# Kernel optimization log

Hardware: AMD Instinct MI355X
Metric: run time of the kernel (lower is better)

## Reference

```python
import jax, jax.numpy as jnp
import numpy as np

D_MODEL = 1024
NUM_HEADS = 16
LOCAL_WINDOW = 128
GLOBAL_STRIDE = 64
B, T = 4, 2048


def _rope_tables(T, d_head, base=10000.0):
    half = d_head // 2
    pos = jnp.arange(T, dtype=jnp.float32)[:, None]
    inv_freq = 1.0 / base ** (jnp.arange(half, dtype=jnp.float32) / half)
    ang = pos * inv_freq[None, :]  # (T, half)
    return jnp.cos(ang), jnp.sin(ang)


def _rope_apply(x, cos_h, sin_h):
    # x: (B, H, T, d_head), cos_h/sin_h: (T, d_head//2); interleaved pairs
    xe = x[..., 0::2]
    xo = x[..., 1::2]
    re = xe * cos_h - xo * sin_h
    ro = xe * sin_h + xo * cos_h
    return jnp.stack([re, ro], axis=-1).reshape(x.shape)


def setup_inputs() -> dict:
    key = jax.random.key(0)
    k1, k2, k3 = jax.random.split(key, 3)
    x = jax.random.normal(k1, (B, T, D_MODEL), dtype=jnp.float32)
    W_qkv = jax.random.normal(k2, (D_MODEL, 3 * D_MODEL), dtype=jnp.float32) * (D_MODEL ** -0.5)
    W_out = jax.random.normal(k3, (D_MODEL, D_MODEL), dtype=jnp.float32) * (D_MODEL ** -0.5)
    b_out = jnp.zeros((D_MODEL,), dtype=jnp.float32)
    return {"x": x, "W_qkv": W_qkv, "W_out": W_out, "b_out": b_out}


def reference(x, W_qkv, W_out, b_out):
    Bx, Tx, C = x.shape
    H = NUM_HEADS
    dh = C // H

    qkv = x @ W_qkv  # (B, T, 3C)
    qkv = qkv.reshape(Bx, Tx, 3, H, dh)
    q, k, v = qkv[:, :, 0], qkv[:, :, 1], qkv[:, :, 2]  # (B, T, H, dh)
    q = jnp.transpose(q, (0, 2, 1, 3))  # (B, H, T, dh)
    k = jnp.transpose(k, (0, 2, 1, 3))
    v = jnp.transpose(v, (0, 2, 1, 3))

    cos_h, sin_h = _rope_tables(Tx, dh)
    q = _rope_apply(q, cos_h, sin_h)
    k = _rope_apply(k, cos_h, sin_h)

    scores = jnp.einsum('bhtd,bhkd->bhtk', q, k) / jnp.sqrt(jnp.float32(dh))

    lw = min(LOCAL_WINDOW, Tx)
    gs = max(1, GLOBAL_STRIDE)
    q_idx = jnp.arange(Tx)
    k_idx = jnp.arange(Tx)
    rel = k_idx[None, :] - q_idx[:, None]  # (T, T)
    local_ok = (rel <= 0) & (rel >= -(lw - 1))
    key_global = (k_idx % gs == 0)[None, :]
    query_is_global = (q_idx % gs == 0)[:, None]
    allowed = (local_ok | key_global | query_is_global) & (rel <= 0)
    allowed = allowed[None, None, :, :]

    scores = jnp.where(allowed, scores, jnp.float32(-1e9))
    w = jax.nn.softmax(scores, axis=-1)
    out = jnp.einsum('bhtk,bhkd->bhtd', w, v)
    out = jnp.transpose(out, (0, 2, 1, 3)).reshape(Bx, Tx, C)
    return out @ W_out + b_out
```

## Files before the change

### kernel.cpp

```cpp
#include <hip/hip_runtime.h>
#include <cstdint>

#define DEV __device__ __forceinline__

typedef __bf16 bf16x8 __attribute__((ext_vector_type(8)));
typedef float f32x4 __attribute__((ext_vector_type(4)));
typedef float f32x16 __attribute__((ext_vector_type(16)));
typedef uint32_t u32x4 __attribute__((ext_vector_type(4)));

DEV uint16_t f2b(float f) {
  uint32_t u = __builtin_bit_cast(uint32_t, f);
  u = u + 0x7fffu + ((u >> 16) & 1u);
  return (uint16_t)(u >> 16);
}
DEV float b2f(uint16_t h) { return __builtin_bit_cast(float, (uint32_t)h << 16); }
DEV uint32_t pk2(float lo, float hi) {
  return (uint32_t)f2b(lo) | ((uint32_t)f2b(hi) << 16);
}

DEV f32x16 mfma32(bf16x8 a, bf16x8 b, f32x16 c) {
  return __builtin_amdgcn_mfma_f32_32x32x16_bf16(a, b, c, 0, 0, 0);
}

DEV void gload16(const void* g, void* s) {
  __builtin_amdgcn_global_load_lds((const __attribute__((address_space(1))) uint32_t*)g,
                                   (__attribute__((address_space(3))) uint32_t*)s, 16, 0, 0);
}

__global__ void k_convert_bf16(const float* __restrict__ X, uint16_t* __restrict__ Xb, int n4) {
  int i = blockIdx.x * 256 + threadIdx.x;
  if (i >= n4) return;
  float4 v = ((const float4*)X)[i];
  uint16_t o0 = f2b(v.x), o1 = f2b(v.y), o2 = f2b(v.z), o3 = f2b(v.w);
  uint64_t packed = (uint64_t)o0 | ((uint64_t)o1 << 16) | ((uint64_t)o2 << 32) | ((uint64_t)o3 << 48);
  ((uint64_t*)Xb)[i] = packed;
}

__global__ __launch_bounds__(256) void k_transpose_bf16(const float* __restrict__ W,
                                                        uint16_t* __restrict__ Wt, int R, int C) {
  __shared__ uint16_t sh[64][68];
  const int tid = threadIdx.x;
  const int bc = blockIdx.x * 64, br = blockIdx.y * 64;
#pragma unroll
  for (int it = 0; it < 16; ++it) {
    const int e = it * 256 + tid;
    const int i = e >> 6, j = e & 63;
    sh[j][i] = f2b(W[(size_t)(br + i) * C + bc + j]);
  }
  __syncthreads();
#pragma unroll
  for (int it = 0; it < 2; ++it) {
    const int e = it * 256 + tid;
    const int j = e >> 3, i8 = (e & 7) * 8;
    uint16_t tmp[8];
#pragma unroll
    for (int k = 0; k < 8; ++k) tmp[k] = sh[j][i8 + k];
    *(uint4*)&Wt[(size_t)(bc + j) * R + br + i8] = *(uint4*)tmp;
  }
}

__global__ void k_rope(float* __restrict__ rc, float* __restrict__ rs) {
  int idx = blockIdx.x * 256 + threadIdx.x;
  if (idx >= 2048 * 32) return;
  int t = idx >> 5, j = idx & 31;
  float inv = powf(10000.f, -(float)j / 32.f);
  float ang = (float)t * inv;
  rc[idx] = cosf(ang);
  rs[idx] = sinf(ang);
}

__global__ __launch_bounds__(256) void k_transpose_v(const uint16_t* __restrict__ V,
                                                     uint16_t* __restrict__ Vt) {
  __shared__ uint16_t sh[64][72];
  const int tid = threadIdx.x;
  const int bh = blockIdx.x >> 5;
  const int t0 = (blockIdx.x & 31) * 64;
#pragma unroll
  for (int it = 0; it < 2; ++it) {
    const int idx = it * 256 + tid;
    const int tr = idx >> 3, d8 = (idx & 7) * 8;
    uint4 vv = *(const uint4*)&V[((size_t)(bh << 11) + t0 + tr) * 64 + d8];
    const uint16_t* e = (const uint16_t*)&vv;
#pragma unroll
    for (int j = 0; j < 8; ++j) sh[d8 + j][tr] = e[j];
  }
  __syncthreads();
#pragma unroll
  for (int it = 0; it < 2; ++it) {
    const int idx = it * 256 + tid;
    const int d = idx >> 3, t8 = (idx & 7) * 8;
    uint16_t tmp[8];
#pragma unroll
    for (int j = 0; j < 8; ++j) tmp[j] = sh[d][t8 + j];
    *(uint4*)&Vt[((size_t)bh * 64 + d) * 2048 + t0 + t8] = *(uint4*)tmp;
  }
}

__global__ __launch_bounds__(256) void k_gather(const uint16_t* __restrict__ Qd,
                                                const uint16_t* __restrict__ Kd,
                                                const uint16_t* __restrict__ Vt,
                                                uint16_t* __restrict__ Qg,
                                                uint16_t* __restrict__ Kg,
                                                uint16_t* __restrict__ Vtg) {
  const int tid = threadIdx.x;
  const int bh = blockIdx.x;
  {
    const int g = tid >> 3, d8 = (tid & 7) * 8;
    const size_t src = ((size_t)(bh << 11) + g * 64) * 64 + d8;
    const size_t dst = ((size_t)bh * 32 + g) * 64 + d8;
    *(uint4*)&Kg[dst] = *(const uint4*)&Kd[src];
    *(uint4*)&Qg[dst] = *(const uint4*)&Qd[src];
  }
  {
    const int d = tid >> 2, g8 = (tid & 3) * 8;
    uint16_t tmp[8];
#pragma unroll
    for (int j = 0; j < 8; ++j) tmp[j] = Vt[((size_t)bh * 64 + d) * 2048 + (size_t)(g8 + j) * 64];
    *(uint4*)&Vtg[((size_t)bh * 64 + d) * 32 + g8] = *(uint4*)tmp;
  }
}

template <int MODE>
__global__ __launch_bounds__(256) void gemm32(
    const uint16_t* __restrict__ A, const uint16_t* __restrict__ Bt,
    int M, int N, int K,
    uint16_t* __restrict__ Qd, uint16_t* __restrict__ Kd, uint16_t* __restrict__ Vd,
    const float* __restrict__ rc, const float* __restrict__ rs,
    float* __restrict__ Cout, const float* __restrict__ bias) {
  __shared__ __align__(16) uint16_t sA[128 * 64];
  __shared__ __align__(16) uint16_t sB[128 * 64];
  const int tid = threadIdx.x;
  const int w = tid >> 6, lane = tid & 63;
  const int wm = w >> 1, wn = w & 1;
  const int ln = lane & 31, hi = lane >> 5;
  const int bm = blockIdx.y * 128, bn = blockIdx.x * 128;

  f32x16 acc[2][2] = {};

  const int lsw = (ln & 7) << 4;

  for (int kt = 0; kt < K; kt += 64) {
#pragma unroll
    for (int r = 0; r < 4; ++r) {
      const int slot = r * 256 + tid;
      const int row = slot >> 3, c8 = slot & 7;
      const int gc = kt + ((c8 ^ (row & 7)) << 3);
      gload16(A + (size_t)(bm + row) * K + gc, (char*)sA + (r * 256 + (tid & ~63)) * 16);
      gload16(Bt + (size_t)(bn + row) * K + gc, (char*)sB + (r * 256 + (tid & ~63)) * 16);
    }
    __syncthreads();
#pragma unroll
    for (int ks = 0; ks < 4; ++ks) {
      const int cb = ks * 32 + hi * 16;
      bf16x8 af[2], bf[2];
#pragma unroll
      for (int mi = 0; mi < 2; ++mi) {
        const int row = wm * 64 + mi * 32 + ln;
        af[mi] = *(const bf16x8*)((const char*)sA + row * 128 + (cb ^ lsw));
      }
#pragma unroll
      for (int ni = 0; ni < 2; ++ni) {
        const int row = wn * 64 + ni * 32 + ln;
        bf[ni] = *(const bf16x8*)((const char*)sB + row * 128 + (cb ^ lsw));
      }
#pragma unroll
      for (int mi = 0; mi < 2; ++mi)
#pragma unroll
        for (int ni = 0; ni < 2; ++ni)
          acc[mi][ni] = mfma32(af[mi], bf[ni], acc[mi][ni]);
    }
    __syncthreads();
  }

#pragma unroll
  for (int mi = 0; mi < 2; ++mi) {
#pragma unroll
    for (int ni = 0; ni < 2; ++ni) {
      const int colb = bn + wn * 64 + ni * 32 + ln;
#pragma unroll
      for (int r = 0; r < 16; ++r) {
        const int crow = (r & 3) + 8 * (r >> 2) + 4 * hi;
        const int row = bm + wm * 64 + mi * 32 + crow;
        float val = acc[mi][ni][r];
        if (MODE == 0) {
          const int b = row >> 11, t = row & 2047;
          const float pv = __shfl_xor(val, 1);
          if (colb < 2048) {
            const int d = colb & 63, j = d >> 1;
            const float c = rc[t * 32 + j], s = rs[t * 32 + j];
            const float rv = (d & 1) ? (val * c + pv * s) : (val * c - pv * s);
            const int cc = colb & 1023, h = cc >> 6;
            uint16_t* dst = (colb < 1024) ? Qd : Kd;
            dst[((((size_t)b * 16 + h) * 2048 + t) << 6) + d] = f2b(rv);
          } else {
            const int cc = colb - 2048;
            const int h = cc >> 6, d = cc & 63;
            Vd[((((size_t)b * 16 + h) * 2048 + t) << 6) + d] = f2b(val);
          }
        } else {
          Cout[(size_t)row * N + colb] = val + bias[colb];
        }
      }
    }
  }
}

template <int MASK>
DEV void attn_tile(const uint16_t* __restrict__ kb_ptr, const uint16_t* __restrict__ v_ptr,
                   const int vrs, const int kb, const int qv, const int hi, const int ln,
                   const bf16x8 qf[4], float& m, float& l, f32x16& acc0, f32x16& acc1) {
  bf16x8 kf0 = *(const bf16x8*)&kb_ptr[ln * 64 + 0 + hi * 8];
  bf16x8 kf1 = *(const bf16x8*)&kb_ptr[ln * 64 + 16 + hi * 8];
  bf16x8 kf2 = *(const bf16x8*)&kb_ptr[ln * 64 + 32 + hi * 8];
  bf16x8 kf3 = *(const bf16x8*)&kb_ptr[ln * 64 + 48 + hi * 8];
  bf16x8 vf00 = *(const bf16x8*)&v_ptr[ln * vrs + hi * 8];
  bf16x8 vf01 = *(const bf16x8*)&v_ptr[ln * vrs + 16 + hi * 8];
  bf16x8 vf10 = *(const bf16x8*)&v_ptr[(32 + ln) * vrs + hi * 8];
  bf16x8 vf11 = *(const bf16x8*)&v_ptr[(32 + ln) * vrs + 16 + hi * 8];

  f32x16 sv = {};
  sv = mfma32(kf0, qf[0], sv);
  sv = mfma32(kf1, qf[1], sv);
  sv = mfma32(kf2, qf[2], sv);
  sv = mfma32(kf3, qf[3], sv);

  float s[16];
  float pm = -3.0e38f;
#pragma unroll
  for (int r = 0; r < 16; ++r) {
    const int crow = (r & 3) + 8 * (r >> 2) + 4 * hi;
    bool ok;
    if (MASK == 0) {
      const int key = kb + crow;
      ok = (key <= qv) && (key + 127 >= qv);
    } else if (MASK == 1) {
      ok = crow * 64 <= qv - 128;
    } else {
      const int key = kb + crow;
      ok = (key <= qv);
    }
    s[r] = ok ? sv[r] * 0.125f : -3.0e38f;
    pm = fmaxf(pm, s[r]);
  }
  pm = fmaxf(pm, __shfl_xor(pm, 32));

  if (__any(pm > m + 8.0f)) {
    const float mn = fmaxf(m, pm);
    const float f = __expf(m - mn);
#pragma unroll
    for (int r = 0; r < 16; ++r) {
      const int crow = (r & 3) + 8 * (r >> 2) + 4 * hi;
      const float fr = __shfl(f, crow);
      acc0[r] *= fr;
      acc1[r] *= fr;
    }
    l *= f;
    m = mn;
  }

  float p[16];
  float ps = 0.f;
#pragma unroll
  for (int r = 0; r < 16; ++r) {
    p[r] = __expf(s[r] - m);
    ps += p[r];
  }
  l += ps + __shfl_xor(ps, 32);

  const uint32_t q0a = pk2(p[0], p[1]), q0b = pk2(p[2], p[3]);
  const uint32_t q1a = pk2(p[4], p[5]), q1b = pk2(p[6], p[7]);
  const uint32_t q2a = pk2(p[8], p[9]), q2b = pk2(p[10], p[11]);
  const uint32_t q3a = pk2(p[12], p[13]), q3b = pk2(p[14], p[15]);
  const uint32_t p0a = __shfl_xor(q0a, 32), p0b = __shfl_xor(q0b, 32);
  const uint32_t p1a = __shfl_xor(q1a, 32), p1b = __shfl_xor(q1b, 32);
  const uint32_t p2a = __shfl_xor(q2a, 32), p2b = __shfl_xor(q2b, 32);
  const uint32_t p3a = __shfl_xor(q3a, 32), p3b = __shfl_xor(q3b, 32);
  u32x4 f0, f1;
  f0[0] = hi ? p1a : q0a; f0[1] = hi ? p1b : q0b; f0[2] = hi ? q1a : p0a; f0[3] = hi ? q1b : p0b;
  f1[0] = hi ? p3a : q2a; f1[1] = hi ? p3b : q2b; f1[2] = hi ? q3a : p2a; f1[3] = hi ? q3b : p2b;
  const bf16x8 pa0 = __builtin_bit_cast(bf16x8, f0);
  const bf16x8 pa1 = __builtin_bit_cast(bf16x8, f1);

  acc0 = mfma32(pa0, vf00, acc0);
  acc0 = mfma32(pa1, vf01, acc0);
  acc1 = mfma32(pa0, vf10, acc1);
  acc1 = mfma32(pa1, vf11, acc1);
}

__global__ __launch_bounds__(256) void attn_main(const uint16_t* __restrict__ Qd,
                                                 const uint16_t* __restrict__ Kd,
                                                 const uint16_t* __restrict__ Vt,
                                                 const uint16_t* __restrict__ Kg,
                                                 const uint16_t* __restrict__ Vtg,
                                                 uint16_t* __restrict__ O) {
  const int tid = threadIdx.x;
  const int wid = blockIdx.x * 4 + (tid >> 6);
  const int bh = wid >> 6, qt = wid & 63;
  const int qb = qt * 32;
  const int lane = tid & 63, hi = lane >> 5, ln = lane & 31;
  const int qv = qb + ln;

  bf16x8 qf[4];
#pragma unroll
  for (int i = 0; i < 4; ++i)
    qf[i] = *(const bf16x8*)&Qd[((size_t)(bh << 11) + qv) * 64 + i * 16 + hi * 8];

  float m = -1e30f, l = 0.f;
  f32x16 acc0 = {}, acc1 = {};

  const int kb0 = qb >= 128 ? qb - 128 : 0;
  for (int kbb = kb0; kbb <= qb; kbb += 32)
    attn_tile<0>(Kd + ((size_t)(bh << 11) + kbb) * 64, Vt + (size_t)bh * 64 * 2048 + kbb, 2048,
                 kbb, qv, hi, ln, qf, m, l, acc0, acc1);
  if (qb >= 128)
    attn_tile<1>(Kg + (size_t)bh * 32 * 64, Vtg + (size_t)bh * 64 * 32, 32,
                 0, qv, hi, ln, qf, m, l, acc0, acc1);

  const float linv = 1.0f / l;
  const int b = bh >> 4, h = bh & 15;
  const int ocol = h * 64 + ln;
#pragma unroll
  for (int r = 0; r < 16; ++r) {
    const int crow = (r & 3) + 8 * (r >> 2) + 4 * hi;
    const float sc = __shfl(linv, crow);
    const size_t orow = (size_t)(b * 2048 + qb + crow);
    O[orow * 1024 + ocol] = f2b(acc0[r] * sc);
    O[orow * 1024 + ocol + 32] = f2b(acc1[r] * sc);
  }
}

__global__ __launch_bounds__(256) void attn_global(const uint16_t* __restrict__ Qg,
                                                   const uint16_t* __restrict__ Kd,
                                                   const uint16_t* __restrict__ Vt,
                                                   uint16_t* __restrict__ O) {
  __shared__ float accL[4][32][64];
  __shared__ float mL[4][32];
  __shared__ float lL[4][32];
  const int tid = threadIdx.x;
  const int bh = blockIdx.x;
  const int wv = tid >> 6, lane = tid & 63, hi = lane >> 5, ln = lane & 31;
  const int qv = ln * 64;

  bf16x8 qf[4];
#pragma unroll
  for (int i = 0; i < 4; ++i)
    qf[i] = *(const bf16x8*)&Qg[((size_t)bh * 32 + ln) * 64 + i * 16 + hi * 8];

  float m = -1e30f, l = 0.f;
  f32x16 acc0 = {}, acc1 = {};
  for (int kt = wv; kt < 64; kt += 4) {
    const int kbb = kt * 32;
    attn_tile<2>(Kd + ((size_t)(bh << 11) + kbb) * 64, Vt + (size_t)bh * 64 * 2048 + kbb, 2048,
                 kbb, qv, hi, ln, qf, m, l, acc0, acc1);
  }

  if (hi == 0) {
    mL[wv][ln] = m;
    lL[wv][ln] = l;
  }
#pragma unroll
  for (int r = 0; r < 16; ++r) {
    const int crow = (r & 3) + 8 * (r >> 2) + 4 * hi;
    accL[wv][crow][ln] = acc0[r];
    accL[wv][crow][ln + 32] = acc1[r];
  }
  __syncthreads();

  const int q = tid >> 3, d0 = (tid & 7) * 8;
  float M = fmaxf(fmaxf(mL[0][q], mL[1][q]), fmaxf(mL[2][q], mL[3][q]));
  float L = 0.f;
  float v[8] = {};
#pragma unroll
  for (int w = 0; w < 4; ++w) {
    const float ew = __expf(mL[w][q] - M);
    L += lL[w][q] * ew;
#pragma unroll
    for (int j = 0; j < 8; ++j) v[j] += accL[w][q][d0 + j] * ew;
  }
  const float Li = 1.0f / L;
  const int b = bh >> 4, h = bh & 15;
  const size_t orow = (size_t)(b * 2048 + q * 64);
#pragma unroll
  for (int j = 0; j < 8; ++j) O[orow * 1024 + h * 64 + d0 + j] = f2b(v[j] * Li);
}

extern "C" void kernel_launch(void* const* d_in, const int* in_sizes, int n_in,
                              void* d_out, int out_size, void* d_ws, size_t ws_size,
                              hipStream_t stream) {
  const float* x = (const float*)d_in[0];
  const float* W_qkv = (const float*)d_in[1];
  const float* W_out = (const float*)d_in[2];
  const float* b_out = (const float*)d_in[3];

  char* ws = (char*)d_ws;
  size_t off = 0;
  auto alloc = [&](size_t bytes) {
    void* p = ws + off;
    off += (bytes + 255) & ~(size_t)255;
    return p;
  };
  uint16_t* xb = (uint16_t*)alloc(8192ull * 1024 * 2);
  uint16_t* wqkvt = (uint16_t*)alloc(3072ull * 1024 * 2);
  uint16_t* woutt = (uint16_t*)alloc(1024ull * 1024 * 2);
  float* rc = (float*)alloc(2048ull * 32 * 4);
  float* rs = (float*)alloc(2048ull * 32 * 4);
  uint16_t* Qd = (uint16_t*)alloc(8192ull * 1024 * 2);
  uint16_t* Kd = (uint16_t*)alloc(8192ull * 1024 * 2);
  uint16_t* Vd = (uint16_t*)alloc(8192ull * 1024 * 2);
  uint16_t* Vt = (uint16_t*)alloc(8192ull * 1024 * 2);
  uint16_t* Qg = (uint16_t*)alloc(64ull * 32 * 64 * 2);
  uint16_t* Kg = (uint16_t*)alloc(64ull * 32 * 64 * 2);
  uint16_t* Vtg = (uint16_t*)alloc(64ull * 64 * 32 * 2);
  uint16_t* O = xb;

  k_convert_bf16<<<8192, 256, 0, stream>>>(x, xb, 8192 * 1024 / 4);
  k_transpose_bf16<<<dim3(48, 16), 256, 0, stream>>>(W_qkv, wqkvt, 1024, 3072);
  k_transpose_bf16<<<dim3(16, 16), 256, 0, stream>>>(W_out, woutt, 1024, 1024);
  k_rope<<<2048 * 32 / 256, 256, 0, stream>>>(rc, rs);

  gemm32<0><<<dim3(24, 64), 256, 0, stream>>>(xb, wqkvt, 8192, 3072, 1024,
                                              Qd, Kd, Vd, rc, rs, nullptr, nullptr);

  k_transpose_v<<<2048, 256, 0, stream>>>(Vd, Vt);
  k_gather<<<64, 256, 0, stream>>>(Qd, Kd, Vt, Qg, Kg, Vtg);

  attn_main<<<1024, 256, 0, stream>>>(Qd, Kd, Vt, Kg, Vtg, O);
  attn_global<<<64, 256, 0, stream>>>(Qg, Kd, Vt, O);

  gemm32<1><<<dim3(8, 64), 256, 0, stream>>>(O, woutt, 8192, 1024, 1024,
                                             nullptr, nullptr, nullptr, nullptr, nullptr,
                                             (float*)d_out, b_out);
}
```

Baseline: 190.1 us.

## Enlarge QKV GEMM M-tile and fuse local and global attention into one launch

The GEMM is templated on the M-tile factor, and the QKV projection now uses 256x128 tiles (MF=4), so each B tile loaded into shared memory feeds twice as many MFMAs. In exchange each block holds more accumulator registers and the grid has fewer blocks. The local-window and global-query attention kernels merge into one launch of 1088 blocks. To keep the two paths from racing on the same output rows, the local path skips writing rows that are global queries. This removes a kernel launch and lets the two workloads overlap.

```diff
diff --git a/kernel.cpp b/kernel.cpp
--- a/kernel.cpp
+++ b/kernel.cpp
@@ -120,42 +120,49 @@
   }
 }
 
-template <int MODE>
-__global__ __launch_bounds__(256) void gemm32(
+template <int MF, int MODE>
+__global__ __launch_bounds__(256) void gemmW(
     const uint16_t* __restrict__ A, const uint16_t* __restrict__ Bt,
     int M, int N, int K,
     uint16_t* __restrict__ Qd, uint16_t* __restrict__ Kd, uint16_t* __restrict__ Vd,
     const float* __restrict__ rc, const float* __restrict__ rs,
     float* __restrict__ Cout, const float* __restrict__ bias) {
-  __shared__ __align__(16) uint16_t sA[128 * 64];
+  constexpr int BM = MF * 64;
+  __shared__ __align__(16) uint16_t sA[BM * 64];
   __shared__ __align__(16) uint16_t sB[128 * 64];
   const int tid = threadIdx.x;
   const int w = tid >> 6, lane = tid & 63;
   const int wm = w >> 1, wn = w & 1;
   const int ln = lane & 31, hi = lane >> 5;
-  const int bm = blockIdx.y * 128, bn = blockIdx.x * 128;
-
-  f32x16 acc[2][2] = {};
+  const int bm = blockIdx.y * BM, bn = blockIdx.x * 128;
+
+  f32x16 acc[MF][2] = {};
 
   const int lsw = (ln & 7) << 4;
 
   for (int kt = 0; kt < K; kt += 64) {
+#pragma unroll
+    for (int r = 0; r < BM / 32; ++r) {
+      const int slot = r * 256 + tid;
+      const int row = slot >> 3, c8 = slot & 7;
+      const int gc = kt + ((c8 ^ (row & 7)) << 3);
+      gload16(A + (size_t)(bm + row) * K + gc, (char*)sA + (r * 256 + (tid & ~63)) * 16);
+    }
 #pragma unroll
     for (int r = 0; r < 4; ++r) {
       const int slot = r * 256 + tid;
       const int row = slot >> 3, c8 = slot & 7;
       const int gc = kt + ((c8 ^ (row & 7)) << 3);
-      gload16(A + (size_t)(bm + row) * K + gc, (char*)sA + (r * 256 + (tid & ~63)) * 16);
       gload16(Bt + (size_t)(bn + row) * K + gc, (char*)sB + (r * 256 + (tid & ~63)) * 16);
     }
     __syncthreads();
 #pragma unroll
     for (int ks = 0; ks < 4; ++ks) {
       const int cb = ks * 32 + hi * 16;
-      bf16x8 af[2], bf[2];
-#pragma unroll
-      for (int mi = 0; mi < 2; ++mi) {
-        const int row = wm * 64 + mi * 32 + ln;
+      bf16x8 af[MF], bf[2];
+#pragma unroll
+      for (int mi = 0; mi < MF; ++mi) {
+        const int row = wm * (MF * 32) + mi * 32 + ln;
         af[mi] = *(const bf16x8*)((const char*)sA + row * 128 + (cb ^ lsw));
       }
 #pragma unroll
@@ -164,7 +171,7 @@
         bf[ni] = *(const bf16x8*)((const char*)sB + row * 128 + (cb ^ lsw));
       }
 #pragma unroll
-      for (int mi = 0; mi < 2; ++mi)
+      for (int mi = 0; mi < MF; ++mi)
 #pragma unroll
         for (int ni = 0; ni < 2; ++ni)
           acc[mi][ni] = mfma32(af[mi], bf[ni], acc[mi][ni]);
@@ -173,14 +180,14 @@
   }
 
 #pragma unroll
-  for (int mi = 0; mi < 2; ++mi) {
+  for (int mi = 0; mi < MF; ++mi) {
 #pragma unroll
     for (int ni = 0; ni < 2; ++ni) {
       const int colb = bn + wn * 64 + ni * 32 + ln;
 #pragma unroll
       for (int r = 0; r < 16; ++r) {
         const int crow = (r & 3) + 8 * (r >> 2) + 4 * hi;
-        const int row = bm + wm * 64 + mi * 32 + crow;
+        const int row = bm + wm * (MF * 32) + mi * 32 + crow;
         float val = acc[mi][ni][r];
         if (MODE == 0) {
           const int b = row >> 11, t = row & 2047;
@@ -287,101 +294,101 @@
   acc1 = mfma32(pa1, vf11, acc1);
 }
 
-__global__ __launch_bounds__(256) void attn_main(const uint16_t* __restrict__ Qd,
-                                                 const uint16_t* __restrict__ Kd,
-                                                 const uint16_t* __restrict__ Vt,
-                                                 const uint16_t* __restrict__ Kg,
-                                                 const uint16_t* __restrict__ Vtg,
-                                                 uint16_t* __restrict__ O) {
-  const int tid = threadIdx.x;
-  const int wid = blockIdx.x * 4 + (tid >> 6);
-  const int bh = wid >> 6, qt = wid & 63;
-  const int qb = qt * 32;
-  const int lane = tid & 63, hi = lane >> 5, ln = lane & 31;
-  const int qv = qb + ln;
-
-  bf16x8 qf[4];
-#pragma unroll
-  for (int i = 0; i < 4; ++i)
-    qf[i] = *(const bf16x8*)&Qd[((size_t)(bh << 11) + qv) * 64 + i * 16 + hi * 8];
-
-  float m = -1e30f, l = 0.f;
-  f32x16 acc0 = {}, acc1 = {};
-
-  const int kb0 = qb >= 128 ? qb - 128 : 0;
-  for (int kbb = kb0; kbb <= qb; kbb += 32)
-    attn_tile<0>(Kd + ((size_t)(bh << 11) + kbb) * 64, Vt + (size_t)bh * 64 * 2048 + kbb, 2048,
-                 kbb, qv, hi, ln, qf, m, l, acc0, acc1);
-  if (qb >= 128)
-    attn_tile<1>(Kg + (size_t)bh * 32 * 64, Vtg + (size_t)bh * 64 * 32, 32,
-                 0, qv, hi, ln, qf, m, l, acc0, acc1);
-
-  const float linv = 1.0f / l;
-  const int b = bh >> 4, h = bh & 15;
-  const int ocol = h * 64 + ln;
-#pragma unroll
-  for (int r = 0; r < 16; ++r) {
-    const int crow = (r & 3) + 8 * (r >> 2) + 4 * hi;
-    const float sc = __shfl(linv, crow);
-    const size_t orow = (size_t)(b * 2048 + qb + crow);
-    O[orow * 1024 + ocol] = f2b(acc0[r] * sc);
-    O[orow * 1024 + ocol + 32] = f2b(acc1[r] * sc);
-  }
-}
-
-__global__ __launch_bounds__(256) void attn_global(const uint16_t* __restrict__ Qg,
-                                                   const uint16_t* __restrict__ Kd,
-                                                   const uint16_t* __restrict__ Vt,
-                                                   uint16_t* __restrict__ O) {
+__global__ __launch_bounds__(256) void attn_fused(const uint16_t* __restrict__ Qd,
+                                                  const uint16_t* __restrict__ Kd,
+                                                  const uint16_t* __restrict__ Vt,
+                                                  const uint16_t* __restrict__ Kg,
+                                                  const uint16_t* __restrict__ Vtg,
+                                                  const uint16_t* __restrict__ Qg,
+                                                  uint16_t* __restrict__ O) {
   __shared__ float accL[4][32][64];
   __shared__ float mL[4][32];
   __shared__ float lL[4][32];
   const int tid = threadIdx.x;
-  const int bh = blockIdx.x;
-  const int wv = tid >> 6, lane = tid & 63, hi = lane >> 5, ln = lane & 31;
-  const int qv = ln * 64;
-
-  bf16x8 qf[4];
-#pragma unroll
-  for (int i = 0; i < 4; ++i)
-    qf[i] = *(const bf16x8*)&Qg[((size_t)bh * 32 + ln) * 64 + i * 16 + hi * 8];
-
-  float m = -1e30f, l = 0.f;
-  f32x16 acc0 = {}, acc1 = {};
-  for (int kt = wv; kt < 64; kt += 4) {
-    const int kbb = kt * 32;
-    attn_tile<2>(Kd + ((size_t)(bh << 11) + kbb) * 64, Vt + (size_t)bh * 64 * 2048 + kbb, 2048,
-                 kbb, qv, hi, ln, qf, m, l, acc0, acc1);
-  }
-
-  if (hi == 0) {
-    mL[wv][ln] = m;
-    lL[wv][ln] = l;
-  }
-#pragma unroll
-  for (int r = 0; r < 16; ++r) {
-    const int crow = (r & 3) + 8 * (r >> 2) + 4 * hi;
-    accL[wv][crow][ln] = acc0[r];
-    accL[wv][crow][ln + 32] = acc1[r];
-  }
-  __syncthreads();
-
-  const int q = tid >> 3, d0 = (tid & 7) * 8;
-  float M = fmaxf(fmaxf(mL[0][q], mL[1][q]), fmaxf(mL[2][q], mL[3][q]));
-  float L = 0.f;
-  float v[8] = {};
-#pragma unroll
-  for (int w = 0; w < 4; ++w) {
-    const float ew = __expf(mL[w][q] - M);
-    L += lL[w][q] * ew;
-#pragma unroll
-    for (int j = 0; j < 8; ++j) v[j] += accL[w][q][d0 + j] * ew;
-  }
-  const float Li = 1.0f / L;
-  const int b = bh >> 4, h = bh & 15;
-  const size_t orow = (size_t)(b * 2048 + q * 64);
-#pragma unroll
-  for (int j = 0; j < 8; ++j) O[orow * 1024 + h * 64 + d0 + j] = f2b(v[j] * Li);
+  const int lane = tid & 63, hi = lane >> 5, ln = lane & 31;
+
+  if (blockIdx.x < 1024) {
+    const int wid = blockIdx.x * 4 + (tid >> 6);
+    const int bh = wid >> 6, qt = wid & 63;
+    const int qb = qt * 32;
+    const int qv = qb + ln;
+
+    bf16x8 qf[4];
+#pragma unroll
+    for (int i = 0; i < 4; ++i)
+      qf[i] = *(const bf16x8*)&Qd[((size_t)(bh << 11) + qv) * 64 + i * 16 + hi * 8];
+
+    float m = -1e30f, l = 0.f;
+    f32x16 acc0 = {}, acc1 = {};
+
+    const int kb0 = qb >= 128 ? qb - 128 : 0;
+    for (int kbb = kb0; kbb <= qb; kbb += 32)
+      attn_tile<0>(Kd + ((size_t)(bh << 11) + kbb) * 64, Vt + (size_t)bh * 64 * 2048 + kbb, 2048,
+                   kbb, qv, hi, ln, qf, m, l, acc0, acc1);
+    if (qb >= 128)
+      attn_tile<1>(Kg + (size_t)bh * 32 * 64, Vtg + (size_t)bh * 64 * 32, 32,
+                   0, qv, hi, ln, qf, m, l, acc0, acc1);
+
+    const float linv = 1.0f / l;
+    const int b = bh >> 4, h = bh & 15;
+    const int ocol = h * 64 + ln;
+    const bool hasg = (qb & 63) == 0;
+#pragma unroll
+    for (int r = 0; r < 16; ++r) {
+      const int crow = (r & 3) + 8 * (r >> 2) + 4 * hi;
+      const float sc = __shfl(linv, crow);
+      if (hasg && crow == 0) continue;
+      const size_t orow = (size_t)(b * 2048 + qb + crow);
+      O[orow * 1024 + ocol] = f2b(acc0[r] * sc);
+      O[orow * 1024 + ocol + 32] = f2b(acc1[r] * sc);
+    }
+  } else {
+    const int bh = blockIdx.x - 1024;
+    const int wv = tid >> 6;
+    const int qv = ln * 64;
+
+    bf16x8 qf[4];
+#pragma unroll
+    for (int i = 0; i < 4; ++i)
+      qf[i] = *(const bf16x8*)&Qg[((size_t)bh * 32 + ln) * 64 + i * 16 + hi * 8];
+
+    float m = -1e30f, l = 0.f;
+    f32x16 acc0 = {}, acc1 = {};
+    for (int kt = wv; kt < 64; kt += 4) {
+      const int kbb = kt * 32;
+      attn_tile<2>(Kd + ((size_t)(bh << 11) + kbb) * 64, Vt + (size_t)bh * 64 * 2048 + kbb, 2048,
+                   kbb, qv, hi, ln, qf, m, l, acc0, acc1);
+    }
+
+    if (hi == 0) {
+      mL[wv][ln] = m;
+      lL[wv][ln] = l;
+    }
+#pragma unroll
+    for (int r = 0; r < 16; ++r) {
+      const int crow = (r & 3) + 8 * (r >> 2) + 4 * hi;
+      accL[wv][crow][ln] = acc0[r];
+      accL[wv][crow][ln + 32] = acc1[r];
+    }
+    __syncthreads();
+
+    const int q = tid >> 3, d0 = (tid & 7) * 8;
+    float M = fmaxf(fmaxf(mL[0][q], mL[1][q]), fmaxf(mL[2][q], mL[3][q]));
+    float L = 0.f;
+    float v[8] = {};
+#pragma unroll
+    for (int w = 0; w < 4; ++w) {
+      const float ew = __expf(mL[w][q] - M);
+      L += lL[w][q] * ew;
+#pragma unroll
+      for (int j = 0; j < 8; ++j) v[j] += accL[w][q][d0 + j] * ew;
+    }
+    const float Li = 1.0f / L;
+    const int b = bh >> 4, h = bh & 15;
+    const size_t orow = (size_t)(b * 2048 + q * 64);
+#pragma unroll
+    for (int j = 0; j < 8; ++j) O[orow * 1024 + h * 64 + d0 + j] = f2b(v[j] * Li);
+  }
 }
 
 extern "C" void kernel_launch(void* const* d_in, const int* in_sizes, int n_in,
@@ -418,16 +425,15 @@
   k_transpose_bf16<<<dim3(16, 16), 256, 0, stream>>>(W_out, woutt, 1024, 1024);
   k_rope<<<2048 * 32 / 256, 256, 0, stream>>>(rc, rs);
 
-  gemm32<0><<<dim3(24, 64), 256, 0, stream>>>(xb, wqkvt, 8192, 3072, 1024,
-                                              Qd, Kd, Vd, rc, rs, nullptr, nullptr);
+  gemmW<4, 0><<<dim3(24, 32), 256, 0, stream>>>(xb, wqkvt, 8192, 3072, 1024,
+                                                Qd, Kd, Vd, rc, rs, nullptr, nullptr);
 
   k_transpose_v<<<2048, 256, 0, stream>>>(Vd, Vt);
   k_gather<<<64, 256, 0, stream>>>(Qd, Kd, Vt, Qg, Kg, Vtg);
 
-  attn_main<<<1024, 256, 0, stream>>>(Qd, Kd, Vt, Kg, Vtg, O);
-  attn_global<<<64, 256, 0, stream>>>(Qg, Kd, Vt, O);
-
-  gemm32<1><<<dim3(8, 64), 256, 0, stream>>>(O, woutt, 8192, 1024, 1024,
-                                             nullptr, nullptr, nullptr, nullptr, nullptr,
-                                             (float*)d_out, b_out);
-}
+  attn_fused<<<1088, 256, 0, stream>>>(Qd, Kd, Vt, Kg, Vtg, Qg, O);
+
+  gemmW<2, 1><<<dim3(8, 64), 256, 0, stream>>>(O, woutt, 8192, 1024, 1024,
+                                               nullptr, nullptr, nullptr, nullptr, nullptr,
+                                               (float*)d_out, b_out);
+}
```

New measurement: 267.0 us. +40.4%, slower.

## Merge local and global attention kernels and enlarge QKV GEMM tile to 256 rows

Applied to the files above, without the earlier changes.

Fuses attn_main and attn_global into one launch: blocks beyond 1024 handle the global query rows, and local blocks skip writing the rows that the global path owns, so the two no longer race on O. The QKV projection GEMM moves to a 256x128 tile with 512 threads, which reuses each B tile across more rows and halves the grid. The goal is to cut a launch and the serial gap between the attention kernels, and to reduce B-operand global traffic. The larger block uses more LDS and registers per CU, which may lower occupancy.

```diff
diff --git a/kernel.cpp b/kernel.cpp
--- a/kernel.cpp
+++ b/kernel.cpp
@@ -120,13 +120,94 @@
   }
 }
 
-template <int MODE>
-__global__ __launch_bounds__(256) void gemm32(
+__global__ __launch_bounds__(512) void gemm256(
     const uint16_t* __restrict__ A, const uint16_t* __restrict__ Bt,
     int M, int N, int K,
     uint16_t* __restrict__ Qd, uint16_t* __restrict__ Kd, uint16_t* __restrict__ Vd,
-    const float* __restrict__ rc, const float* __restrict__ rs,
-    float* __restrict__ Cout, const float* __restrict__ bias) {
+    const float* __restrict__ rc, const float* __restrict__ rs) {
+  __shared__ __align__(16) uint16_t sA[256 * 64];
+  __shared__ __align__(16) uint16_t sB[128 * 64];
+  const int tid = threadIdx.x;
+  const int w = tid >> 6, lane = tid & 63;
+  const int wm = w >> 1, wn = w & 1;
+  const int ln = lane & 31, hi = lane >> 5;
+  const int bm = blockIdx.y * 256, bn = blockIdx.x * 128;
+
+  f32x16 acc[2][2] = {};
+
+  const int lsw = (ln & 7) << 4;
+
+  for (int kt = 0; kt < K; kt += 64) {
+#pragma unroll
+    for (int r = 0; r < 4; ++r) {
+      const int slot = r * 512 + tid;
+      const int row = slot >> 3, c8 = slot & 7;
+      const int gc = kt + ((c8 ^ (row & 7)) << 3);
+      gload16(A + (size_t)(bm + row) * K + gc, (char*)sA + (r * 512 + (tid & ~63)) * 16);
+    }
+#pragma unroll
+    for (int r = 0; r < 2; ++r) {
+      const int slot = r * 512 + tid;
+      const int row = slot >> 3, c8 = slot & 7;
+      const int gc = kt + ((c8 ^ (row & 7)) << 3);
+      gload16(Bt + (size_t)(bn + row) * K + gc, (char*)sB + (r * 512 + (tid & ~63)) * 16);
+    }
+    __syncthreads();
+#pragma unroll
+    for (int ks = 0; ks < 4; ++ks) {
+      const int cb = ks * 32 + hi * 16;
+      bf16x8 af[2], bf[2];
+#pragma unroll
+      for (int mi = 0; mi < 2; ++mi) {
+        const int row = wm * 64 + mi * 32 + ln;
+        af[mi] = *(const bf16x8*)((const char*)sA + row * 128 + (cb ^ lsw));
+      }
+#pragma unroll
+      for (int ni = 0; ni < 2; ++ni) {
+        const int row = wn * 64 + ni * 32 + ln;
+        bf[ni] = *(const bf16x8*)((const char*)sB + row * 128 + (cb ^ lsw));
+      }
+#pragma unroll
+      for (int mi = 0; mi < 2; ++mi)
+#pragma unroll
+        for (int ni = 0; ni < 2; ++ni)
+          acc[mi][ni] = mfma32(af[mi], bf[ni], acc[mi][ni]);
+    }
+    __syncthreads();
+  }
+
+#pragma unroll
+  for (int mi = 0; mi < 2; ++mi) {
+#pragma unroll
+    for (int ni = 0; ni < 2; ++ni) {
+      const int colb = bn + wn * 64 + ni * 32 + ln;
+#pragma unroll
+      for (int r = 0; r < 16; ++r) {
+        const int crow = (r & 3) + 8 * (r >> 2) + 4 * hi;
+        const int row = bm + wm * 64 + mi * 32 + crow;
+        float val = acc[mi][ni][r];
+        const int b = row >> 11, t = row & 2047;
+        const float pv = __shfl_xor(val, 1);
+        if (colb < 2048) {
+          const int d = colb & 63, j = d >> 1;
+          const float c = rc[t * 32 + j], s = rs[t * 32 + j];
+          const float rv = (d & 1) ? (val * c + pv * s) : (val * c - pv * s);
+          const int cc = colb & 1023, h = cc >> 6;
+          uint16_t* dst = (colb < 1024) ? Qd : Kd;
+          dst[((((size_t)b * 16 + h) * 2048 + t) << 6) + d] = f2b(rv);
+        } else {
+          const int cc = colb - 2048;
+          const int h = cc >> 6, d = cc & 63;
+          Vd[((((size_t)b * 16 + h) * 2048 + t) << 6) + d] = f2b(val);
+        }
+      }
+    }
+  }
+}
+
+__global__ __launch_bounds__(256) void gemm128(
+    const uint16_t* __restrict__ A, const uint16_t* __restrict__ Bt,
+    int M, int N, int K, float* __restrict__ Cout, const float* __restrict__ bias) {
   __shared__ __align__(16) uint16_t sA[128 * 64];
   __shared__ __align__(16) uint16_t sB[128 * 64];
   const int tid = threadIdx.x;
@@ -136,7 +217,6 @@
   const int bm = blockIdx.y * 128, bn = blockIdx.x * 128;
 
   f32x16 acc[2][2] = {};
-
   const int lsw = (ln & 7) << 4;
 
   for (int kt = 0; kt < K; kt += 64) {
@@ -181,25 +261,7 @@
       for (int r = 0; r < 16; ++r) {
         const int crow = (r & 3) + 8 * (r >> 2) + 4 * hi;
         const int row = bm + wm * 64 + mi * 32 + crow;
-        float val = acc[mi][ni][r];
-        if (MODE == 0) {
-          const int b = row >> 11, t = row & 2047;
-          const float pv = __shfl_xor(val, 1);
-          if (colb < 2048) {
-            const int d = colb & 63, j = d >> 1;
-            const float c = rc[t * 32 + j], s = rs[t * 32 + j];
-            const float rv = (d & 1) ? (val * c + pv * s) : (val * c - pv * s);
-            const int cc = colb & 1023, h = cc >> 6;
-            uint16_t* dst = (colb < 1024) ? Qd : Kd;
-            dst[((((size_t)b * 16 + h) * 2048 + t) << 6) + d] = f2b(rv);
-          } else {
-            const int cc = colb - 2048;
-            const int h = cc >> 6, d = cc & 63;
-            Vd[((((size_t)b * 16 + h) * 2048 + t) << 6) + d] = f2b(val);
-          }
-        } else {
-          Cout[(size_t)row * N + colb] = val + bias[colb];
-        }
+        Cout[(size_t)row * N + colb] = acc[mi][ni][r] + bias[colb];
       }
     }
   }
@@ -287,101 +349,101 @@
   acc1 = mfma32(pa1, vf11, acc1);
 }
 
-__global__ __launch_bounds__(256) void attn_main(const uint16_t* __restrict__ Qd,
-                                                 const uint16_t* __restrict__ Kd,
-                                                 const uint16_t* __restrict__ Vt,
-                                                 const uint16_t* __restrict__ Kg,
-                                                 const uint16_t* __restrict__ Vtg,
-                                                 uint16_t* __restrict__ O) {
-  const int tid = threadIdx.x;
-  const int wid = blockIdx.x * 4 + (tid >> 6);
-  const int bh = wid >> 6, qt = wid & 63;
-  const int qb = qt * 32;
-  const int lane = tid & 63, hi = lane >> 5, ln = lane & 31;
-  const int qv = qb + ln;
-
-  bf16x8 qf[4];
-#pragma unroll
-  for (int i = 0; i < 4; ++i)
-    qf[i] = *(const bf16x8*)&Qd[((size_t)(bh << 11) + qv) * 64 + i * 16 + hi * 8];
-
-  float m = -1e30f, l = 0.f;
-  f32x16 acc0 = {}, acc1 = {};
-
-  const int kb0 = qb >= 128 ? qb - 128 : 0;
-  for (int kbb = kb0; kbb <= qb; kbb += 32)
-    attn_tile<0>(Kd + ((size_t)(bh << 11) + kbb) * 64, Vt + (size_t)bh * 64 * 2048 + kbb, 2048,
-                 kbb, qv, hi, ln, qf, m, l, acc0, acc1);
-  if (qb >= 128)
-    attn_tile<1>(Kg + (size_t)bh * 32 * 64, Vtg + (size_t)bh * 64 * 32, 32,
-                 0, qv, hi, ln, qf, m, l, acc0, acc1);
-
-  const float linv = 1.0f / l;
-  const int b = bh >> 4, h = bh & 15;
-  const int ocol = h * 64 + ln;
-#pragma unroll
-  for (int r = 0; r < 16; ++r) {
-    const int crow = (r & 3) + 8 * (r >> 2) + 4 * hi;
-    const float sc = __shfl(linv, crow);
-    const size_t orow = (size_t)(b * 2048 + qb + crow);
-    O[orow * 1024 + ocol] = f2b(acc0[r] * sc);
-    O[orow * 1024 + ocol + 32] = f2b(acc1[r] * sc);
-  }
-}
-
-__global__ __launch_bounds__(256) void attn_global(const uint16_t* __restrict__ Qg,
-                                                   const uint16_t* __restrict__ Kd,
-                                                   const uint16_t* __restrict__ Vt,
-                                                   uint16_t* __restrict__ O) {
+__global__ __launch_bounds__(256) void attn_fused(const uint16_t* __restrict__ Qd,
+                                                  const uint16_t* __restrict__ Kd,
+                                                  const uint16_t* __restrict__ Vt,
+                                                  const uint16_t* __restrict__ Kg,
+                                                  const uint16_t* __restrict__ Vtg,
+                                                  const uint16_t* __restrict__ Qg,
+                                                  uint16_t* __restrict__ O) {
   __shared__ float accL[4][32][64];
   __shared__ float mL[4][32];
   __shared__ float lL[4][32];
   const int tid = threadIdx.x;
-  const int bh = blockIdx.x;
-  const int wv = tid >> 6, lane = tid & 63, hi = lane >> 5, ln = lane & 31;
-  const int qv = ln * 64;
-
-  bf16x8 qf[4];
-#pragma unroll
-  for (int i = 0; i < 4; ++i)
-    qf[i] = *(const bf16x8*)&Qg[((size_t)bh * 32 + ln) * 64 + i * 16 + hi * 8];
-
-  float m = -1e30f, l = 0.f;
-  f32x16 acc0 = {}, acc1 = {};
-  for (int kt = wv; kt < 64; kt += 4) {
-    const int kbb = kt * 32;
-    attn_tile<2>(Kd + ((size_t)(bh << 11) + kbb) * 64, Vt + (size_t)bh * 64 * 2048 + kbb, 2048,
-                 kbb, qv, hi, ln, qf, m, l, acc0, acc1);
-  }
-
-  if (hi == 0) {
-    mL[wv][ln] = m;
-    lL[wv][ln] = l;
-  }
-#pragma unroll
-  for (int r = 0; r < 16; ++r) {
-    const int crow = (r & 3) + 8 * (r >> 2) + 4 * hi;
-    accL[wv][crow][ln] = acc0[r];
-    accL[wv][crow][ln + 32] = acc1[r];
-  }
-  __syncthreads();
-
-  const int q = tid >> 3, d0 = (tid & 7) * 8;
-  float M = fmaxf(fmaxf(mL[0][q], mL[1][q]), fmaxf(mL[2][q], mL[3][q]));
-  float L = 0.f;
-  float v[8] = {};
-#pragma unroll
-  for (int w = 0; w < 4; ++w) {
-    const float ew = __expf(mL[w][q] - M);
-    L += lL[w][q] * ew;
-#pragma unroll
-    for (int j = 0; j < 8; ++j) v[j] += accL[w][q][d0 + j] * ew;
-  }
-  const float Li = 1.0f / L;
-  const int b = bh >> 4, h = bh & 15;
-  const size_t orow = (size_t)(b * 2048 + q * 64);
-#pragma unroll
-  for (int j = 0; j < 8; ++j) O[orow * 1024 + h * 64 + d0 + j] = f2b(v[j] * Li);
+  const int lane = tid & 63, hi = lane >> 5, ln = lane & 31;
+
+  if (blockIdx.x < 1024) {
+    const int wid = blockIdx.x * 4 + (tid >> 6);
+    const int bh = wid >> 6, qt = wid & 63;
+    const int qb = qt * 32;
+    const int qv = qb + ln;
+
+    bf16x8 qf[4];
+#pragma unroll
+    for (int i = 0; i < 4; ++i)
+      qf[i] = *(const bf16x8*)&Qd[((size_t)(bh << 11) + qv) * 64 + i * 16 + hi * 8];
+
+    float m = -1e30f, l = 0.f;
+    f32x16 acc0 = {}, acc1 = {};
+
+    const int kb0 = qb >= 128 ? qb - 128 : 0;
+    for (int kbb = kb0; kbb <= qb; kbb += 32)
+      attn_tile<0>(Kd + ((size_t)(bh << 11) + kbb) * 64, Vt + (size_t)bh * 64 * 2048 + kbb, 2048,
+                   kbb, qv, hi, ln, qf, m, l, acc0, acc1);
+    if (qb >= 128)
+      attn_tile<1>(Kg + (size_t)bh * 32 * 64, Vtg + (size_t)bh * 64 * 32, 32,
+                   0, qv, hi, ln, qf, m, l, acc0, acc1);
+
+    const float linv = 1.0f / l;
+    const int b = bh >> 4, h = bh & 15;
+    const int ocol = h * 64 + ln;
+    const bool hasg = (qb & 63) == 0;
+#pragma unroll
+    for (int r = 0; r < 16; ++r) {
+      const int crow = (r & 3) + 8 * (r >> 2) + 4 * hi;
+      const float sc = __shfl(linv, crow);
+      if (hasg && crow == 0) continue;
+      const size_t orow = (size_t)(b * 2048 + qb + crow);
+      O[orow * 1024 + ocol] = f2b(acc0[r] * sc);
+      O[orow * 1024 + ocol + 32] = f2b(acc1[r] * sc);
+    }
+  } else {
+    const int bh = blockIdx.x - 1024;
+    const int wv = tid >> 6;
+    const int qv = ln * 64;
+
+    bf16x8 qf[4];
+#pragma unroll
+    for (int i = 0; i < 4; ++i)
+      qf[i] = *(const bf16x8*)&Qg[((size_t)bh * 32 + ln) * 64 + i * 16 + hi * 8];
+
+    float m = -1e30f, l = 0.f;
+    f32x16 acc0 = {}, acc1 = {};
+    for (int kt = wv; kt < 64; kt += 4) {
+      const int kbb = kt * 32;
+      attn_tile<2>(Kd + ((size_t)(bh << 11) + kbb) * 64, Vt + (size_t)bh * 64 * 2048 + kbb, 2048,
+                   kbb, qv, hi, ln, qf, m, l, acc0, acc1);
+    }
+
+    if (hi == 0) {
+      mL[wv][ln] = m;
+      lL[wv][ln] = l;
+    }
+#pragma unroll
+    for (int r = 0; r < 16; ++r) {
+      const int crow = (r & 3) + 8 * (r >> 2) + 4 * hi;
+      accL[wv][crow][ln] = acc0[r];
+      accL[wv][crow][ln + 32] = acc1[r];
+    }
+    __syncthreads();
+
+    const int q = tid >> 3, d0 = (tid & 7) * 8;
+    float M = fmaxf(fmaxf(mL[0][q], mL[1][q]), fmaxf(mL[2][q], mL[3][q]));
+    float L = 0.f;
+    float v[8] = {};
+#pragma unroll
+    for (int w = 0; w < 4; ++w) {
+      const float ew = __expf(mL[w][q] - M);
+      L += lL[w][q] * ew;
+#pragma unroll
+      for (int j = 0; j < 8; ++j) v[j] += accL[w][q][d0 + j] * ew;
+    }
+    const float Li = 1.0f / L;
+    const int b = bh >> 4, h = bh & 15;
+    const size_t orow = (size_t)(b * 2048 + q * 64);
+#pragma unroll
+    for (int j = 0; j < 8; ++j) O[orow * 1024 + h * 64 + d0 + j] = f2b(v[j] * Li);
+  }
 }
 
 extern "C" void kernel_launch(void* const* d_in, const int* in_sizes, int n_in,
@@ -418,16 +480,14 @@
   k_transpose_bf16<<<dim3(16, 16), 256, 0, stream>>>(W_out, woutt, 1024, 1024);
   k_rope<<<2048 * 32 / 256, 256, 0, stream>>>(rc, rs);
 
-  gemm32<0><<<dim3(24, 64), 256, 0, stream>>>(xb, wqkvt, 8192, 3072, 1024,
-                                              Qd, Kd, Vd, rc, rs, nullptr, nullptr);
+  gemm256<<<dim3(24, 32), 512, 0, stream>>>(xb, wqkvt, 8192, 3072, 1024,
+                                            Qd, Kd, Vd, rc, rs);
 
   k_transpose_v<<<2048, 256, 0, stream>>>(Vd, Vt);
   k_gather<<<64, 256, 0, stream>>>(Qd, Kd, Vt, Qg, Kg, Vtg);
 
-  attn_main<<<1024, 256, 0, stream>>>(Qd, Kd, Vt, Kg, Vtg, O);
-  attn_global<<<64, 256, 0, stream>>>(Qg, Kd, Vt, O);
-
-  gemm32<1><<<dim3(8, 64), 256, 0, stream>>>(O, woutt, 8192, 1024, 1024,
-                                             nullptr, nullptr, nullptr, nullptr, nullptr,
-                                             (float*)d_out, b_out);
-}
+  attn_fused<<<1088, 256, 0, stream>>>(Qd, Kd, Vt, Kg, Vtg, Qg, O);
+
+  gemm128<<<dim3(8, 64), 256, 0, stream>>>(O, woutt, 8192, 1024, 1024,
+                                           (float*)d_out, b_out);
+}
```

Result: slower. 195.3 us (+2.7%).
